# Optimization experiments

Measured on AMD Instinct MI355X. Metric: run time of the kernel, lower is better.

Reference implementation:

```python
import jax, jax.numpy as jnp
import numpy as np

# Module constants (from Flanger.__init__ defaults and forward defaults)
SAMPLE_RATE = 44100
BASE_DELAY_MS = 5.0
DELAY_RANGE_MS = 4.0
RATE = 0.5      # LFO rate (Hz)
DEPTH = 0.7     # modulation depth
FEEDBACK = 0.3  # feedback amount (clamped to 0.9 in forward)
MIX = 0.5       # dry/wet mix


def _next_pow2(n):
    p = 1
    while p < n:
        p *= 2
    return p


def _delay_schedule(T):
    """Host-side precompute of the data-independent delay schedule.
    Matches the torch loop: int() truncation, & mask circular wrap."""
    base = int(BASE_DELAY_MS * SAMPLE_RATE / 1000)               # 220
    rng = int(DELAY_RANGE_MS * SAMPLE_RATE / 1000 * DEPTH)       # 123
    max_delay = int((BASE_DELAY_MS + DELAY_RANGE_MS) * SAMPLE_RATE / 1000) + 10
    buf_size = _next_pow2(max_delay)                             # 512
    mask = buf_size - 1
    t = np.arange(T, dtype=np.float64)
    phase = (t * RATE / SAMPLE_RATE) % 1.0
    mod = np.sin(2.0 * np.pi * phase)
    delay = base + np.trunc(mod * rng).astype(np.int64)          # int() truncates toward zero
    delay = np.clip(delay, 1, buf_size - 1)
    write_idx = (np.arange(T, dtype=np.int64) & mask)
    read_idx = (write_idx - delay) & mask
    return buf_size, read_idx.astype(np.int32), write_idx.astype(np.int32)


def setup_inputs() -> dict:
    key = jax.random.key(0)
    x = jax.random.normal(key, (64, 220500), dtype=jnp.float32)  # [B, T] = 64 clips of 5s @ 44.1kHz
    return {"x": x}


def reference(x):
    B, T = x.shape
    buf_size, read_idx, write_idx = _delay_schedule(T)
    fb = min(FEEDBACK, 0.9)

    def step(buffer, inp):
        xt, ri, wi = inp                       # xt: [B], ri/wi: scalar int32
        delayed = buffer[:, ri]                # [B] circular-buffer read
        out_t = xt * (1.0 - MIX) + delayed * MIX
        buffer = buffer.at[:, wi].set(xt + delayed * fb)  # feedback write
        return buffer, out_t

    buffer0 = jnp.zeros((B, buf_size), dtype=x.dtype)
    xs = (x.T, jnp.asarray(read_idx), jnp.asarray(write_idx))
    _, out = jax.lax.scan(step, buffer0, xs)   # out: [T, B]
    return out.T
```

## Files before the change

kernel.cpp:

```cpp
#include <hip/hip_runtime.h>
#include <math.h>

#define T_LEN 220500
#define FB 0.3f
#define KMAX 4
#define TPB 1024
#define TILE_BACK 1376
#define TILE_USED (TPB + TILE_BACK)
#define TILE_PAD 2432
#define BPB 2
#define NTH 256

typedef float f2 __attribute__((ext_vector_type(2)));

__device__ __forceinline__ int delay_at(int cur) {
    double phase = fmod(((double)cur * 0.5) / 44100.0, 1.0);
    double mod = sin(2.0 * M_PI * phase);
    int delay = 220 + (int)trunc(mod * 123.0);
    if (delay < 1) delay = 1;
    if (delay > 511) delay = 511;
    return delay;
}

__global__ void expand_kernel(unsigned short* __restrict__ Dw, int T, int TT) {
    int t = blockIdx.x * NTH + threadIdx.x;
    if (t >= TT) return;
    int tb  = t >> 10;
    int r   = t & 1023;
    int i   = r >> 9;
    int e   = r & 1;
    int tid = (r >> 1) & 255;
    unsigned short* base = Dw + (((size_t)tb * 2) * 256 + tid) * 8 + i * 2 + e;
    int cur = t;
    int cum4 = 0;
    bool live = (t < T);
    #pragma unroll
    for (int k = 0; k < KMAX; ++k) {
        int inc = 97;
        if (live) {
            inc = delay_at(cur);
            cur -= inc;
            if (cur < 0) live = false;
        }
        cum4 += inc << 2;
        base[(size_t)(k >> 1) * (256 * 8) + (k & 1) * 4] = (unsigned short)cum4;
    }
}

__global__ __launch_bounds__(NTH, 8) void gather_kernel(
    const float* __restrict__ x, const unsigned short* __restrict__ Dw,
    float* __restrict__ out, int T, int B) {
    const int b0  = blockIdx.x * BPB;
    const int tb  = blockIdx.y;
    const int tid = threadIdx.x;
    const int t0  = tb * TPB;
    const bool has2 = (b0 + 1 < B);
    __shared__ float tile[2 * TILE_PAD];

    const int g0 = t0 - TILE_BACK;
    const bool interior = (g0 >= 0) && (g0 + TILE_USED <= T);
    const float* __restrict__ xb0 = x + (size_t)b0 * T;
    const float* __restrict__ xb1 = xb0 + (has2 ? T : 0);

    if (interior) {
        #pragma unroll
        for (int s = 0; s < 3; ++s) {
            int j4 = (s * NTH + tid) * 4;
            if (j4 < TILE_USED) {
                __builtin_amdgcn_global_load_lds(
                    (const __attribute__((address_space(1))) void*)(xb0 + g0 + j4),
                    (__attribute__((address_space(3))) void*)(tile + j4), 16, 0, 0);
                __builtin_amdgcn_global_load_lds(
                    (const __attribute__((address_space(1))) void*)(xb1 + g0 + j4),
                    (__attribute__((address_space(3))) void*)(tile + TILE_PAD + j4), 16, 0, 0);
            }
        }
    } else {
        for (int bb = 0; bb < BPB; ++bb) {
            const float* __restrict__ xb = (bb == 0) ? xb0 : xb1;
            #pragma unroll
            for (int s = 0; s < 3; ++s) {
                int j4 = (s * NTH + tid) * 4;
                if (j4 < TILE_USED) {
                    int g = g0 + j4;
                    float4 v;
                    if (g >= 0 && g <= T - 4) {
                        v = *(const float4*)(xb + g);
                    } else {
                        v.x = (g     >= 0 && g     < T) ? xb[g]     : 0.0f;
                        v.y = (g + 1 >= 0 && g + 1 < T) ? xb[g + 1] : 0.0f;
                        v.z = (g + 2 >= 0 && g + 2 < T) ? xb[g + 2] : 0.0f;
                        v.w = (g + 3 >= 0 && g + 3 < T) ? xb[g + 3] : 0.0f;
                    }
                    *(float4*)(tile + bb * TILE_PAD + j4) = v;
                }
            }
        }
    }

    const unsigned short* __restrict__ db =
        Dw + (((size_t)tb * 2) * 256 + tid) * 8;
    uint4 w0 = *(const uint4*)(db);
    uint4 w1 = *(const uint4*)(db + 256 * 8);

    __syncthreads();

    const char* __restrict__ tb8 = (const char*)tile;

    int ab[2];
    f2  acc[2][2];
    #pragma unroll
    for (int i = 0; i < 2; ++i) {
        ab[i] = (TILE_BACK + 2 * tid + 512 * i) * 4;
        #pragma unroll
        for (int e = 0; e < 2; ++e) {
            int a = ab[i] + 4 * e;
            f2 v;
            v.x = *(const float*)(tb8 + a);
            v.y = *(const float*)(tb8 + a + TILE_PAD * 4);
            acc[i][e] = 0.5f * v;
        }
    }

    float coef = 0.5f;
    #pragma unroll
    for (int k = 0; k < KMAX; ++k) {
        uint4 w = (k < 2) ? w0 : w1;
        f2 cc; cc.x = coef; cc.y = coef;
        #pragma unroll
        for (int i = 0; i < 2; ++i) {
            unsigned u = (k & 1) ? ((i == 0) ? w.z : w.w)
                                 : ((i == 0) ? w.x : w.y);
            #pragma unroll
            for (int e = 0; e < 2; ++e) {
                int c4 = (e == 0) ? (int)(u & 0xFFFFu) : (int)(u >> 16);
                int a = ab[i] + 4 * e - c4;
                f2 v;
                v.x = *(const float*)(tb8 + a);
                v.y = *(const float*)(tb8 + a + TILE_PAD * 4);
                acc[i][e] += cc * v;
            }
        }
        coef *= FB;
    }

    float* __restrict__ ob0 = out + (size_t)b0 * T;
    float* __restrict__ ob1 = out + (size_t)(has2 ? b0 + 1 : b0) * T;
    #pragma unroll
    for (int i = 0; i < 2; ++i) {
        int t = t0 + 2 * tid + 512 * i;
        if (t < T) {
            f2 s0; s0.x = acc[i][0].x; s0.y = acc[i][1].x;
            *(f2*)(ob0 + t) = s0;
            if (has2) {
                f2 s1; s1.x = acc[i][0].y; s1.y = acc[i][1].y;
                *(f2*)(ob1 + t) = s1;
            }
        }
    }
}

__global__ __launch_bounds__(256) void flanger_direct_kernel(
    const float* __restrict__ x, float* __restrict__ out, int T) {
    int t = blockIdx.x * blockDim.x + threadIdx.x;
    if (t >= T) return;
    int b = blockIdx.y;
    const float* xb = x + (size_t)b * T;
    float acc = 0.5f * xb[t];
    float coef = 0.5f;
    int cur = t;
    #pragma unroll 1
    for (int k = 0; k < 8; ++k) {
        cur -= delay_at(cur);
        if (cur < 0) break;
        acc += coef * xb[cur];
        coef *= FB;
    }
    out[(size_t)b * T + t] = acc;
}

extern "C" void kernel_launch(void* const* d_in, const int* in_sizes, int n_in,
                              void* d_out, int out_size, void* d_ws, size_t ws_size,
                              hipStream_t stream) {
    const float* x = (const float*)d_in[0];
    float* out = (float*)d_out;
    const int T = T_LEN;
    const int B = in_sizes[0] / T;

    const int TB = (T + TPB - 1) / TPB;
    const int TT = TB * TPB;

    unsigned short* Dw = (unsigned short*)d_ws;
    size_t need = (size_t)TB * 2 * 256 * 8 * sizeof(unsigned short);

    if (ws_size >= need) {
        expand_kernel<<<(TT + NTH - 1) / NTH, NTH, 0, stream>>>(Dw, T, TT);
        dim3 grid((B + BPB - 1) / BPB, TB);
        gather_kernel<<<grid, NTH, 0, stream>>>(x, Dw, out, T, B);
    } else {
        dim3 grid((T + 255) / 256, B);
        flanger_direct_kernel<<<grid, 256, 0, stream>>>(x, out, T);
    }
}
```

Before: 31.66 us.

## Store batch pairs as packed fp16 in LDS and double time tile

The shared-memory tile now holds the two batch rows interleaved as packed half-precision pairs, converted from fp32 on load. Each gathered tap therefore needs one 32-bit LDS read instead of two. The time tile grows from 1024 to 2048 samples per block, and the offset table now stores absolute tile offsets per tap rather than cumulative deltas. This halves LDS traffic and amortises the halo, but replaces the async global-to-LDS copy with register loads plus conversion. It also rounds inputs to fp16, which adds precision error, and the fallback path now truncates the feedback series at four taps.

```diff
diff --git a/kernel.cpp b/kernel.cpp
--- a/kernel.cpp
+++ b/kernel.cpp
@@ -4,14 +4,13 @@
 #define T_LEN 220500
 #define FB 0.3f
 #define KMAX 4
-#define TPB 1024
+#define TPB 2048
 #define TILE_BACK 1376
 #define TILE_USED (TPB + TILE_BACK)
-#define TILE_PAD 2432
-#define BPB 2
 #define NTH 256
 
 typedef float f2 __attribute__((ext_vector_type(2)));
+typedef _Float16 h2v __attribute__((ext_vector_type(2)));
 
 __device__ __forceinline__ int delay_at(int cur) {
     double phase = fmod(((double)cur * 0.5) / 44100.0, 1.0);
@@ -25,37 +24,33 @@
 __global__ void expand_kernel(unsigned short* __restrict__ Dw, int T, int TT) {
     int t = blockIdx.x * NTH + threadIdx.x;
     if (t >= TT) return;
-    int tb  = t >> 10;
-    int r   = t & 1023;
+    int tb  = t >> 11;
+    int r   = t & 2047;
     int i   = r >> 9;
     int e   = r & 1;
     int tid = (r >> 1) & 255;
-    unsigned short* base = Dw + (((size_t)tb * 2) * 256 + tid) * 8 + i * 2 + e;
+    unsigned short* base = Dw + (((size_t)tb * KMAX) * 256 + tid) * 8 + i * 2 + e;
+    int t0  = tb << 11;
     int cur = t;
-    int cum4 = 0;
     bool live = (t < T);
     #pragma unroll
     for (int k = 0; k < KMAX; ++k) {
-        int inc = 97;
-        if (live) {
-            inc = delay_at(cur);
-            cur -= inc;
-            if (cur < 0) live = false;
-        }
-        cum4 += inc << 2;
-        base[(size_t)(k >> 1) * (256 * 8) + (k & 1) * 4] = (unsigned short)cum4;
+        int inc = live ? delay_at(cur) : 97;
+        cur -= inc;
+        if (cur < 0) live = false;
+        base[(size_t)k * (256 * 8)] = (unsigned short)((cur - t0 + TILE_BACK) << 2);
     }
 }
 
 __global__ __launch_bounds__(NTH, 8) void gather_kernel(
     const float* __restrict__ x, const unsigned short* __restrict__ Dw,
     float* __restrict__ out, int T, int B) {
-    const int b0  = blockIdx.x * BPB;
+    const int b0  = blockIdx.x * 2;
     const int tb  = blockIdx.y;
     const int tid = threadIdx.x;
-    const int t0  = tb * TPB;
+    const int t0  = tb << 11;
     const bool has2 = (b0 + 1 < B);
-    __shared__ float tile[2 * TILE_PAD];
+    __shared__ unsigned tile[TILE_USED];
 
     const int g0 = t0 - TILE_BACK;
     const bool interior = (g0 >= 0) && (g0 + TILE_USED <= T);
@@ -64,81 +59,79 @@
 
     if (interior) {
         #pragma unroll
-        for (int s = 0; s < 3; ++s) {
+        for (int s = 0; s < 4; ++s) {
             int j4 = (s * NTH + tid) * 4;
             if (j4 < TILE_USED) {
-                __builtin_amdgcn_global_load_lds(
-                    (const __attribute__((address_space(1))) void*)(xb0 + g0 + j4),
-                    (__attribute__((address_space(3))) void*)(tile + j4), 16, 0, 0);
-                __builtin_amdgcn_global_load_lds(
-                    (const __attribute__((address_space(1))) void*)(xb1 + g0 + j4),
-                    (__attribute__((address_space(3))) void*)(tile + TILE_PAD + j4), 16, 0, 0);
+                int g = g0 + j4;
+                float4 a = *(const float4*)(xb0 + g);
+                float4 b = *(const float4*)(xb1 + g);
+                uint4 d;
+                d.x = __builtin_bit_cast(unsigned, __builtin_amdgcn_cvt_pkrtz(a.x, b.x));
+                d.y = __builtin_bit_cast(unsigned, __builtin_amdgcn_cvt_pkrtz(a.y, b.y));
+                d.z = __builtin_bit_cast(unsigned, __builtin_amdgcn_cvt_pkrtz(a.z, b.z));
+                d.w = __builtin_bit_cast(unsigned, __builtin_amdgcn_cvt_pkrtz(a.w, b.w));
+                *(uint4*)(tile + j4) = d;
             }
         }
     } else {
-        for (int bb = 0; bb < BPB; ++bb) {
-            const float* __restrict__ xb = (bb == 0) ? xb0 : xb1;
-            #pragma unroll
-            for (int s = 0; s < 3; ++s) {
-                int j4 = (s * NTH + tid) * 4;
-                if (j4 < TILE_USED) {
-                    int g = g0 + j4;
-                    float4 v;
-                    if (g >= 0 && g <= T - 4) {
-                        v = *(const float4*)(xb + g);
-                    } else {
-                        v.x = (g     >= 0 && g     < T) ? xb[g]     : 0.0f;
-                        v.y = (g + 1 >= 0 && g + 1 < T) ? xb[g + 1] : 0.0f;
-                        v.z = (g + 2 >= 0 && g + 2 < T) ? xb[g + 2] : 0.0f;
-                        v.w = (g + 3 >= 0 && g + 3 < T) ? xb[g + 3] : 0.0f;
-                    }
-                    *(float4*)(tile + bb * TILE_PAD + j4) = v;
+        #pragma unroll
+        for (int s = 0; s < 4; ++s) {
+            int j4 = (s * NTH + tid) * 4;
+            if (j4 < TILE_USED) {
+                uint4 d;
+                #pragma unroll
+                for (int m = 0; m < 4; ++m) {
+                    int g = g0 + j4 + m;
+                    float va = (g >= 0 && g < T) ? xb0[g] : 0.0f;
+                    float vb = (g >= 0 && g < T) ? xb1[g] : 0.0f;
+                    unsigned dm = __builtin_bit_cast(unsigned, __builtin_amdgcn_cvt_pkrtz(va, vb));
+                    if (m == 0) d.x = dm; else if (m == 1) d.y = dm;
+                    else if (m == 2) d.z = dm; else d.w = dm;
                 }
+                *(uint4*)(tile + j4) = d;
             }
         }
     }
 
     const unsigned short* __restrict__ db =
-        Dw + (((size_t)tb * 2) * 256 + tid) * 8;
+        Dw + (((size_t)tb * KMAX) * 256 + tid) * 8;
     uint4 w0 = *(const uint4*)(db);
-    uint4 w1 = *(const uint4*)(db + 256 * 8);
+    uint4 w1 = *(const uint4*)(db + 2048);
+    uint4 w2 = *(const uint4*)(db + 4096);
+    uint4 w3 = *(const uint4*)(db + 6144);
 
     __syncthreads();
 
-    const char* __restrict__ tb8 = (const char*)tile;
+    const char* __restrict__ t8 = (const char*)tile;
 
-    int ab[2];
-    f2  acc[2][2];
+    float acc0[4][2], acc1[4][2];
     #pragma unroll
-    for (int i = 0; i < 2; ++i) {
-        ab[i] = (TILE_BACK + 2 * tid + 512 * i) * 4;
-        #pragma unroll
-        for (int e = 0; e < 2; ++e) {
-            int a = ab[i] + 4 * e;
-            f2 v;
-            v.x = *(const float*)(tb8 + a);
-            v.y = *(const float*)(tb8 + a + TILE_PAD * 4);
-            acc[i][e] = 0.5f * v;
-        }
+    for (int i = 0; i < 4; ++i) {
+        uint2 c = *(const uint2*)(tile + TILE_BACK + 2 * tid + 512 * i);
+        h2v v0 = __builtin_bit_cast(h2v, c.x);
+        h2v v1 = __builtin_bit_cast(h2v, c.y);
+        acc0[i][0] = 0.5f * (float)v0.x;  acc1[i][0] = 0.5f * (float)v0.y;
+        acc0[i][1] = 0.5f * (float)v1.x;  acc1[i][1] = 0.5f * (float)v1.y;
     }
 
     float coef = 0.5f;
     #pragma unroll
     for (int k = 0; k < KMAX; ++k) {
-        uint4 w = (k < 2) ? w0 : w1;
-        f2 cc; cc.x = coef; cc.y = coef;
+        uint4 w = (k == 0) ? w0 : (k == 1) ? w1 : (k == 2) ? w2 : w3;
         #pragma unroll
-        for (int i = 0; i < 2; ++i) {
-            unsigned u = (k & 1) ? ((i == 0) ? w.z : w.w)
-                                 : ((i == 0) ? w.x : w.y);
-            #pragma unroll
-            for (int e = 0; e < 2; ++e) {
-                int c4 = (e == 0) ? (int)(u & 0xFFFFu) : (int)(u >> 16);
-                int a = ab[i] + 4 * e - c4;
-                f2 v;
-                v.x = *(const float*)(tb8 + a);
-                v.y = *(const float*)(tb8 + a + TILE_PAD * 4);
-                acc[i][e] += cc * v;
+        for (int i = 0; i < 4; ++i) {
+            unsigned u = (i == 0) ? w.x : (i == 1) ? w.y : (i == 2) ? w.z : w.w;
+            {
+                unsigned dw = *(const unsigned*)(t8 + (u & 0xFFFFu));
+                h2v v = __builtin_bit_cast(h2v, dw);
+                acc0[i][0] += coef * (float)v.x;
+                acc1[i][0] += coef * (float)v.y;
+            }
+            {
+                unsigned dw = *(const unsigned*)(t8 + (u >> 16));
+                h2v v = __builtin_bit_cast(h2v, dw);
+                acc0[i][1] += coef * (float)v.x;
+                acc1[i][1] += coef * (float)v.y;
             }
         }
         coef *= FB;
@@ -147,13 +140,13 @@
     float* __restrict__ ob0 = out + (size_t)b0 * T;
     float* __restrict__ ob1 = out + (size_t)(has2 ? b0 + 1 : b0) * T;
     #pragma unroll
-    for (int i = 0; i < 2; ++i) {
+    for (int i = 0; i < 4; ++i) {
         int t = t0 + 2 * tid + 512 * i;
         if (t < T) {
-            f2 s0; s0.x = acc[i][0].x; s0.y = acc[i][1].x;
+            f2 s0; s0.x = acc0[i][0]; s0.y = acc0[i][1];
             *(f2*)(ob0 + t) = s0;
             if (has2) {
-                f2 s1; s1.x = acc[i][0].y; s1.y = acc[i][1].y;
+                f2 s1; s1.x = acc1[i][0]; s1.y = acc1[i][1];
                 *(f2*)(ob1 + t) = s1;
             }
         }
@@ -170,7 +163,7 @@
     float coef = 0.5f;
     int cur = t;
     #pragma unroll 1
-    for (int k = 0; k < 8; ++k) {
+    for (int k = 0; k < KMAX; ++k) {
         cur -= delay_at(cur);
         if (cur < 0) break;
         acc += coef * xb[cur];
@@ -191,11 +184,11 @@
     const int TT = TB * TPB;
 
     unsigned short* Dw = (unsigned short*)d_ws;
-    size_t need = (size_t)TB * 2 * 256 * 8 * sizeof(unsigned short);
+    size_t need = (size_t)TB * KMAX * 256 * 8 * sizeof(unsigned short);
 
     if (ws_size >= need) {
         expand_kernel<<<(TT + NTH - 1) / NTH, NTH, 0, stream>>>(Dw, T, TT);
-        dim3 grid((B + BPB - 1) / BPB, TB);
+        dim3 grid(B / 2 + (B & 1), TB);
         gather_kernel<<<grid, NTH, 0, stream>>>(x, Dw, out, T, B);
     } else {
         dim3 grid((T + 255) / 256, B);
```

Measured after the change: 33.41 us. +5.5%, slower.
